# Kernel tuning notes

Hardware: AMD Instinct MI355X
Metric: run time of the kernel (lower is better)

## Reference

```python
import jax, jax.numpy as jnp
import numpy as np

B, F, DIM = 32, 2048, 1024
H, DH, Q, DEPTH, MULT = 16, 64, 64, 6, 2
INNER = H * DH  # 1024
EPS = 1e-5


def _ln(x, g, b):
    m = jnp.mean(x, axis=-1, keepdims=True)
    v = jnp.mean((x - m) ** 2, axis=-1, keepdims=True)
    return (x - m) / jnp.sqrt(v + EPS) * g + b


def setup_inputs() -> dict:
    key = jax.random.key(0)
    ks = iter(jax.random.split(key, 32))
    def rn(shape, s=0.02):
        return jax.random.normal(next(ks), shape, dtype=jnp.float32) * s
    inp = {
        "features": jax.random.normal(next(ks), (B, F, DIM), dtype=jnp.float32),
        "mask": jax.random.randint(next(ks), (B, F), 0, 2),
        "latents": jax.random.normal(next(ks), (Q, INNER), dtype=jnp.float32),
        "W_down": rn((DIM, INNER)),
        "nin_g": jnp.ones((DIM,)), "nin_b": jnp.zeros((DIM,)),
        "lf_g": jnp.ones((DEPTH, INNER)), "lf_b": jnp.zeros((DEPTH, INNER)),
        "ll_g": jnp.ones((DEPTH, INNER)), "ll_b": jnp.zeros((DEPTH, INNER)),
        "Wq": rn((DEPTH, INNER, INNER)),
        "Wk": rn((DEPTH, INNER, INNER)),
        "Wv": rn((DEPTH, INNER, INNER)),
        "ffln_g": jnp.ones((DEPTH, INNER)), "ffln_b": jnp.zeros((DEPTH, INNER)),
        "ff_w1": rn((DEPTH, INNER, MULT * INNER)),
        "ff_w2": rn((DEPTH, MULT * INNER, INNER)),
        "nout_g": jnp.ones((INNER,)), "nout_b": jnp.zeros((INNER,)),
    }
    return inp


def reference(features, mask, latents, W_down, nin_g, nin_b, lf_g, lf_b, ll_g, ll_b,
              Wq, Wk, Wv, ffln_g, ffln_b, ff_w1, ff_w2, nout_g, nout_b):
    scale = DH ** (-0.5)
    # input norm + projection down to inner_dim
    f = _ln(features, nin_g, nin_b) @ W_down            # (B, F, INNER)
    x = jnp.broadcast_to(latents, (B, Q, INNER))        # (B, Q, INNER)
    keep = (mask != 0)[:, None, None, :]                # (B, 1, 1, F)
    for i in range(DEPTH):
        xf = _ln(f, lf_g[i], lf_b[i])
        xl = _ln(x, ll_g[i], ll_b[i])
        q = (xl @ Wq[i]).reshape(B, Q, H, DH).transpose(0, 2, 1, 3) * scale  # bhqd
        k = (xf @ Wk[i]).reshape(B, F, H, DH).transpose(0, 2, 1, 3)          # bhfd
        v = (xf @ Wv[i]).reshape(B, F, H, DH).transpose(0, 2, 1, 3)          # bhfd
        sim = jnp.einsum('bhqd,bhfd->bhqf', q, k)
        sim = sim - jax.lax.stop_gradient(jnp.max(sim, axis=-1, keepdims=True))
        sim = jnp.where(keep, sim, -jnp.inf)
        alphas = jax.nn.softmax(sim, axis=-1)
        alphas = jnp.nan_to_num(alphas, nan=0.0)        # fully-masked rows -> 0
        out = jnp.einsum('bhqf,bhfd->bqhd', alphas, v).reshape(B, Q, INNER)
        # feed-forward: LN -> Linear -> ReLU -> Linear
        h = jax.nn.relu(_ln(out, ffln_g[i], ffln_b[i]) @ ff_w1[i]) @ ff_w2[i]
        x = x + h
    return _ln(x, nout_g, nout_b)
```

## Files before the change

kernel.cpp:

```cpp
#include <hip/hip_runtime.h>
#include <stdint.h>


#define DEV static __device__ __forceinline__

typedef __attribute__((ext_vector_type(8))) short short8;
typedef __attribute__((ext_vector_type(4))) float f32x4;
typedef __attribute__((ext_vector_type(4))) int int4v;
typedef __attribute__((ext_vector_type(4))) unsigned short ushort4v;
typedef unsigned short ushort_t;

DEV float bf2f(ushort_t u){ union{uint32_t i; float f;} x; x.i = ((uint32_t)u)<<16; return x.f; }
DEV ushort_t f2bf(float f){
  union{float f; uint32_t i;} x; x.f = f;
  uint32_t r = x.i + 0x7fffu + ((x.i>>16)&1u);
  return (ushort_t)(r>>16);
}

#define GLOAD16(gp, lp) __builtin_amdgcn_global_load_lds( \
    (const __attribute__((address_space(1))) uint32_t*)(gp), \
    (__attribute__((address_space(3))) uint32_t*)(lp), 16, 0, 0)

#define VMCNT(n) asm volatile("s_waitcnt vmcnt(" #n ")" ::: "memory")
#define CFENCE   asm volatile("" ::: "memory")
#define MFMA16(a,b,c) __builtin_amdgcn_mfma_f32_16x16x32_bf16(a,b,c,0,0,0)
#define MFMAI8(a,b,c) __builtin_amdgcn_mfma_i32_16x16x64_i8(a,b,c,0,0,0)

template<int NXB>
DEV void xcd_remapN(int g, int total, int& x, int& y){
  int xcd = g & 7;
  int k = g >> 3;
  int rows_per_xcd = (total / NXB) >> 3;
  y = xcd * rows_per_xcd + (k / NXB);
  x = k % NXB;
}

DEV void wreduce2(float& a, float& b){
  #pragma unroll
  for (int d = 32; d; d >>= 1){ a += __shfl_xor(a, d); b += __shfl_xor(b, d); }
}

__global__ __launch_bounds__(256) void k_compact(const int* __restrict__ mask,
                                                 int* __restrict__ idx, int* __restrict__ cnt){
  int b = blockIdx.x, t = threadIdx.x;
  const int* mb = mask + b*2048;
  int keep[8]; int c = 0;
  #pragma unroll
  for (int u = 0; u < 8; ++u){ keep[u] = (mb[t*8+u] != 0); c += keep[u]; }
  __shared__ int s[256];
  s[t] = c; __syncthreads();
  for (int off = 1; off < 256; off <<= 1){
    int v = (t >= off) ? s[t-off] : 0;
    __syncthreads();
    s[t] += v;
    __syncthreads();
  }
  int pos = s[t] - c;
  #pragma unroll
  for (int u = 0; u < 8; ++u) if (keep[u]) idx[b*2048 + pos++] = t*8 + u;
  if (t == 255) cnt[b] = s[255];
}

__global__ __launch_bounds__(256) void k_gather_norm(const float* __restrict__ feat,
        const int* __restrict__ idx, const int* __restrict__ cnt, ushort_t* __restrict__ outp){
  int w = threadIdx.x >> 6, l = threadIdx.x & 63;
  int row = blockIdx.x*4 + w;
  int b = row >> 11, j = row & 2047;
  if (j >= cnt[b]) return;
  int src = idx[b*2048 + j];
  const float* rp = feat + ((size_t)(b*2048 + src))*1024;
  float4 v[4]; float s = 0.f, q = 0.f;
  #pragma unroll
  for (int i = 0; i < 4; ++i){
    v[i] = *(const float4*)(rp + i*256 + l*4);
    s += v[i].x+v[i].y+v[i].z+v[i].w;
    q += v[i].x*v[i].x+v[i].y*v[i].y+v[i].z*v[i].z+v[i].w*v[i].w;
  }
  wreduce2(s, q);
  float mean = s * (1.f/1024.f);
  float rstd = rsqrtf(q*(1.f/1024.f) - mean*mean + 1e-5f);
  ushort_t* op = outp + (size_t)row*1024;
  #pragma unroll
  for (int i = 0; i < 4; ++i){
    ushort4v o;
    o.x = f2bf((v[i].x-mean)*rstd); o.y = f2bf((v[i].y-mean)*rstd);
    o.z = f2bf((v[i].z-mean)*rstd); o.w = f2bf((v[i].w-mean)*rstd);
    *(ushort4v*)(op + i*256 + l*4) = o;
  }
}

__global__ __launch_bounds__(256) void k_rownorm_i8(const ushort_t* __restrict__ in,
        int8_t* __restrict__ outp, float* __restrict__ sca, const int* __restrict__ cnt){
  int w = threadIdx.x >> 6, l = threadIdx.x & 63;
  int row = blockIdx.x*4 + w;
  if (cnt){ int b = row >> 11; if ((row & 2047) >= cnt[b]) return; }
  const ushort_t* rp = in + (size_t)row*1024 + l*16;
  float f[16]; float s = 0.f, q = 0.f;
  #pragma unroll
  for (int i = 0; i < 4; ++i){
    ushort4v u = *(const ushort4v*)(rp + i*4);
    f[i*4+0] = bf2f(u.x); f[i*4+1] = bf2f(u.y);
    f[i*4+2] = bf2f(u.z); f[i*4+3] = bf2f(u.w);
  }
  #pragma unroll
  for (int jj = 0; jj < 16; ++jj){ s += f[jj]; q += f[jj]*f[jj]; }
  wreduce2(s, q);
  float mean = s * (1.f/1024.f);
  float rstd = rsqrtf(q*(1.f/1024.f) - mean*mean + 1e-5f);
  float amax = 0.f;
  #pragma unroll
  for (int jj = 0; jj < 16; ++jj) amax = fmaxf(amax, fabsf(f[jj]-mean));
  #pragma unroll
  for (int d = 32; d; d >>= 1) amax = fmaxf(amax, __shfl_xor(amax, d));
  amax *= rstd;
  float inv = (amax > 0.f) ? 127.f/amax : 0.f;
  if (l == 0) sca[row] = amax * (1.f/127.f);
  uint32_t wds[4];
  #pragma unroll
  for (int i = 0; i < 4; ++i){
    uint32_t wd = 0;
    #pragma unroll
    for (int c = 0; c < 4; ++c){
      int qv = (int)rintf((f[i*4+c]-mean)*rstd*inv);
      wd |= ((uint32_t)(uint8_t)(int8_t)qv) << (c*8);
    }
    wds[i] = wd;
  }
  int4v pk; pk[0]=(int)wds[0]; pk[1]=(int)wds[1]; pk[2]=(int)wds[2]; pk[3]=(int)wds[3];
  *(int4v*)(outp + (size_t)row*1024 + l*16) = pk;
}

__global__ __launch_bounds__(256) void k_rownorm_f32_i8(const float* __restrict__ in,
        int8_t* __restrict__ outp, float* __restrict__ sca){
  int w = threadIdx.x >> 6, l = threadIdx.x & 63;
  int row = blockIdx.x*4 + w;
  const float* rp = in + (size_t)row*1024 + l*16;
  float f[16]; float s = 0.f, q = 0.f;
  #pragma unroll
  for (int i = 0; i < 4; ++i){
    float4 v = *(const float4*)(rp + i*4);
    f[i*4+0] = v.x; f[i*4+1] = v.y; f[i*4+2] = v.z; f[i*4+3] = v.w;
  }
  #pragma unroll
  for (int jj = 0; jj < 16; ++jj){ s += f[jj]; q += f[jj]*f[jj]; }
  wreduce2(s, q);
  float mean = s * (1.f/1024.f);
  float rstd = rsqrtf(q*(1.f/1024.f) - mean*mean + 1e-5f);
  float amax = 0.f;
  #pragma unroll
  for (int jj = 0; jj < 16; ++jj) amax = fmaxf(amax, fabsf(f[jj]-mean));
  #pragma unroll
  for (int d = 32; d; d >>= 1) amax = fmaxf(amax, __shfl_xor(amax, d));
  amax *= rstd;
  float inv = (amax > 0.f) ? 127.f/amax : 0.f;
  if (l == 0) sca[row] = amax * (1.f/127.f);
  uint32_t wds[4];
  #pragma unroll
  for (int i = 0; i < 4; ++i){
    uint32_t wd = 0;
    #pragma unroll
    for (int c = 0; c < 4; ++c){
      int qv = (int)rintf((f[i*4+c]-mean)*rstd*inv);
      wd |= ((uint32_t)(uint8_t)(int8_t)qv) << (c*8);
    }
    wds[i] = wd;
  }
  int4v pk; pk[0]=(int)wds[0]; pk[1]=(int)wds[1]; pk[2]=(int)wds[2]; pk[3]=(int)wds[3];
  *(int4v*)(outp + (size_t)row*1024 + l*16) = pk;
}

template<int PER>
__global__ __launch_bounds__(256) void k_quant_rows(const ushort_t* __restrict__ in,
        int8_t* __restrict__ outp, float* __restrict__ sca){
  const int K = PER*64;
  int w = threadIdx.x >> 6, l = threadIdx.x & 63;
  int row = blockIdx.x*4 + w;
  const ushort_t* rp = in + (size_t)row*K + l*PER;
  float f[PER];
  #pragma unroll
  for (int i = 0; i < PER/4; ++i){
    ushort4v u = *(const ushort4v*)(rp + i*4);
    f[i*4+0] = bf2f(u.x); f[i*4+1] = bf2f(u.y);
    f[i*4+2] = bf2f(u.z); f[i*4+3] = bf2f(u.w);
  }
  float amax = 0.f;
  #pragma unroll
  for (int jj = 0; jj < PER; ++jj) amax = fmaxf(amax, fabsf(f[jj]));
  #pragma unroll
  for (int d = 32; d; d >>= 1) amax = fmaxf(amax, __shfl_xor(amax, d));
  float inv = (amax > 0.f) ? 127.f/amax : 0.f;
  if (l == 0) sca[row] = amax * (1.f/127.f);
  #pragma unroll
  for (int vq = 0; vq < PER/16; ++vq){
    int4v pk;
    #pragma unroll
    for (int i = 0; i < 4; ++i){
      uint32_t wd = 0;
      #pragma unroll
      for (int c = 0; c < 4; ++c){
        int qv = (int)rintf(f[vq*16 + i*4 + c]*inv);
        wd |= ((uint32_t)(uint8_t)(int8_t)qv) << (c*8);
      }
      pk[i] = (int)wd;
    }
    *(int4v*)(outp + (size_t)row*K + l*PER + vq*16) = pk;
  }
}

__global__ __launch_bounds__(256) void k_final_ln(const float* __restrict__ x,
        const float* __restrict__ g, const float* __restrict__ bb, float* __restrict__ outp){
  int w = threadIdx.x >> 6, l = threadIdx.x & 63;
  int row = blockIdx.x*4 + w;
  const float* rp = x + (size_t)row*1024;
  float4 v[4]; float s = 0.f, q = 0.f;
  #pragma unroll
  for (int i = 0; i < 4; ++i){
    v[i] = *(const float4*)(rp + i*256 + l*4);
    s += v[i].x+v[i].y+v[i].z+v[i].w;
    q += v[i].x*v[i].x+v[i].y*v[i].y+v[i].z*v[i].z+v[i].w*v[i].w;
  }
  wreduce2(s, q);
  float mean = s * (1.f/1024.f);
  float rstd = rsqrtf(q*(1.f/1024.f) - mean*mean + 1e-5f);
  float* op = outp + (size_t)row*1024;
  #pragma unroll
  for (int i = 0; i < 4; ++i){
    float4 gg = *(const float4*)(g + i*256 + l*4);
    float4 bv = *(const float4*)(bb + i*256 + l*4);
    float4 o;
    o.x = (v[i].x-mean)*rstd*gg.x + bv.x; o.y = (v[i].y-mean)*rstd*gg.y + bv.y;
    o.z = (v[i].z-mean)*rstd*gg.z + bv.z; o.w = (v[i].w-mean)*rstd*gg.w + bv.w;
    *(float4*)(op + i*256 + l*4) = o;
  }
}

__global__ __launch_bounds__(256) void k_init_x(const float* __restrict__ lat, float* __restrict__ x){
  int v = blockIdx.x*256 + threadIdx.x;
  int row = v >> 8, cv = v & 255;
  ((float4*)x)[v] = ((const float4*)lat)[(row & 63)*256 + cv];
}

DEV void foldT_body(const float* __restrict__ W, const float* __restrict__ g,
                    float scale, ushort_t* __restrict__ Wt, int K, int N,
                    int n0, int k0){
  __shared__ float Ts[64][65];
  int t = threadIdx.x;
  #pragma unroll
  for (int i = 0; i < 4; ++i){
    int flat = i*1024 + t*4; int r = flat >> 6, c = flat & 63;
    float4 v = *(const float4*)(W + (size_t)(k0+r)*N + n0 + c);
    float gg = (g ? g[k0+r] : 1.f) * scale;
    Ts[r][c] = v.x*gg; Ts[r][c+1] = v.y*gg; Ts[r][c+2] = v.z*gg; Ts[r][c+3] = v.w*gg;
  }
  __syncthreads();
  #pragma unroll
  for (int i = 0; i < 4; ++i){
    int flat = i*1024 + t*4; int rn = flat >> 6, ck = flat & 63;
    ushort4v o;
    o.x = f2bf(Ts[ck][rn]);   o.y = f2bf(Ts[ck+1][rn]);
    o.z = f2bf(Ts[ck+2][rn]); o.w = f2bf(Ts[ck+3][rn]);
    *(ushort4v*)(Wt + (size_t)(n0+rn)*K + k0 + ck) = o;
  }
}

struct FDesc { const float* W; const float* g; ushort_t* dst; float scale; int K; int N; };
#define MAXFD 32
struct FoldTArgs { int cnt; FDesc d[MAXFD]; };

__global__ __launch_bounds__(256) void k_foldT_all(FoldTArgs a){
  const FDesc d = a.d[blockIdx.y];
  int nxb = d.N >> 6;
  int n0 = (blockIdx.x % nxb) * 64;
  int k0 = (blockIdx.x / nxb) * 64;
  if (k0 >= d.K) return;
  foldT_body(d.W, d.g, d.scale, d.dst, d.K, d.N, n0, k0);
}

DEV void foldBias_body(const float* __restrict__ W, const float* __restrict__ bvec,
                       float scale, float* __restrict__ bias, int K, int N, int o0){
  int t = threadIdx.x;
  int ol = t & 31, kc = t >> 5;
  int o = o0 + ol;
  int chunk = K >> 3;
  int c0 = kc*chunk, c1 = c0 + chunk;
  float s0 = 0, s1 = 0, s2 = 0, s3 = 0;
  for (int c = c0; c < c1; c += 4){
    s0 += bvec[c+0]*W[(size_t)(c+0)*N + o];
    s1 += bvec[c+1]*W[(size_t)(c+1)*N + o];
    s2 += bvec[c+2]*W[(size_t)(c+2)*N + o];
    s3 += bvec[c+3]*W[(size_t)(c+3)*N + o];
  }
  __shared__ float red[8][32];
  red[kc][ol] = (s0+s1)+(s2+s3);
  __syncthreads();
  if (kc == 0){
    float tot = 0;
    #pragma unroll
    for (int jj = 0; jj < 8; ++jj) tot += red[jj][ol];
    bias[o] = tot * scale;
  }
}

struct BDesc { const float* W; const float* b; float* dst; float scale; int K; int N; };
#define MAXBD 25
struct BiasArgs { int cnt; BDesc d[MAXBD]; };

__global__ __launch_bounds__(256) void k_foldBias_all(BiasArgs a){
  const BDesc d = a.d[blockIdx.y];
  int o0 = blockIdx.x * 32;
  if (o0 >= d.N) return;
  foldBias_body(d.W, d.b, d.scale, d.dst, d.K, d.N, o0);
}

template<int OUTMODE>
__global__ __launch_bounds__(256, 4) void k_gemm128i8(const int8_t* __restrict__ A,
        const int8_t* __restrict__ Bt, const float* __restrict__ sAr,
        const float* __restrict__ sBr, const float* __restrict__ bias,
        void* __restrict__ Cp, int M, int N, int Kb){
  const int n0 = blockIdx.x * 128;
  const int m0 = blockIdx.y * 128;
  __shared__ __align__(16) char sA[2][128*64];
  __shared__ __align__(16) char sB[2][128*64];
  const int tid = threadIdx.x;
  const int wave = tid >> 6, lane = tid & 63;
  const int lo = lane & 15, hi = lane >> 4;
  const int wr = wave >> 1, wc = wave & 1;

  auto stage = [&](int buf, int k0){
    #pragma unroll
    for (int p = 0; p < 2; ++p){
      int r = p*64 + wave*16 + (lane >> 2);
      int c = lane & 3;
      {
        const int8_t* gp = A + (size_t)(m0 + r)*Kb + k0 + c*16;
        char* lp = (char*)(&sA[buf][0]) + p*4096 + wave*1024;
        GLOAD16(gp, lp);
      }
      {
        const int8_t* gp = Bt + (size_t)(n0 + r)*Kb + k0 + c*16;
        char* lp = (char*)(&sB[buf][0]) + p*4096 + wave*1024;
        GLOAD16(gp, lp);
      }
    }
  };

  int4v acc[4][4] = {};
  stage(0, 0);
  const int nk = Kb >> 6;
  for (int ks = 0; ks < nk; ++ks){
    __syncthreads();
    if (ks + 1 < nk) stage((ks+1)&1, (ks+1) << 6);
    const int buf = ks & 1;
    int4v af[4], bfr[4];
    #pragma unroll
    for (int mi = 0; mi < 4; ++mi)
      af[mi] = *(const int4v*)(&sA[buf][(wr*64 + mi*16 + lo)*64 + hi*16]);
    #pragma unroll
    for (int ni = 0; ni < 4; ++ni)
      bfr[ni] = *(const int4v*)(&sB[buf][(wc*64 + ni*16 + lo)*64 + hi*16]);
    #pragma unroll
    for (int mi = 0; mi < 4; ++mi)
      #pragma unroll
      for (int ni = 0; ni < 4; ++ni)
        acc[mi][ni] = MFMAI8(af[mi], bfr[ni], acc[mi][ni]);
  }
  #pragma unroll
  for (int ni = 0; ni < 4; ++ni){
    int col = n0 + wc*64 + ni*16 + lo;
    float bv = bias ? bias[col] : 0.f;
    float sb = sBr[col];
    #pragma unroll
    for (int mi = 0; mi < 4; ++mi){
      int rbase = m0 + wr*64 + mi*16 + hi*4;
      #pragma unroll
      for (int rr = 0; rr < 4; ++rr){
        int row = rbase + rr;
        float v = (float)acc[mi][ni][rr] * (sAr[row]*sb) + bv;
        size_t off = (size_t)row*N + col;
        if (OUTMODE == 0)      ((ushort_t*)Cp)[off] = f2bf(v);
        else if (OUTMODE == 1) ((ushort_t*)Cp)[off] = f2bf(fmaxf(v, 0.f));
        else                   ((float*)Cp)[off] += v;
      }
    }
  }
}

template<bool SKIP, int NXB>
__global__ __launch_bounds__(512, 2) void k_gemm256p8(const ushort_t* __restrict__ A,
        const ushort_t* __restrict__ Bt, const float* __restrict__ bias,
        ushort_t* __restrict__ Cp, int M, int N, int K, const int* __restrict__ cnt){
  int bx, by;
  xcd_remapN<NXB>(blockIdx.x, gridDim.x, bx, by);
  const int n0 = bx * 256;
  const int m0 = by * 256;
  if (SKIP){ int b = m0 >> 11; if ((m0 & 2047) >= cnt[b]) return; }
  __shared__ __align__(16) ushort_t sA[2][256*64];
  __shared__ __align__(16) ushort_t sB[2][256*64];
  const int tid = threadIdx.x;
  const int wave = tid >> 6, lane = tid & 63;
  const int lo = lane & 15, hi = lane >> 4;
  const int wm = wave >> 2, wn = wave & 3;
  const int srow = lane >> 3;
  const int schunk = (lane & 7) ^ srow;
  auto stageHalf = [&](ushort_t* dst, const ushort_t* __restrict__ G, int grow0,
                       int half, int k0){
    #pragma unroll
    for (int p = 0; p < 2; ++p){
      int rbase = half*128 + p*64 + wave*8;
      const ushort_t* gp = G + (size_t)(grow0 + rbase + srow)*K + k0 + schunk*8;
      char* lp = (char*)dst + (size_t)rbase*128;
      GLOAD16(gp, lp);
    }
  };
  auto ldsA = [&](int buf, int row, int kk)->short8{
    int ch = ((kk<<2) + hi) ^ (row & 7);
    return *(const short8*)((const char*)sA + (size_t)buf*32768 + (size_t)row*128 + ch*16);
  };
  auto ldsB = [&](int buf, int row, int kk)->short8{
    int ch = ((kk<<2) + hi) ^ (row & 7);
    return *(const short8*)((const char*)sB + (size_t)buf*32768 + (size_t)row*128 + ch*16);
  };
  f32x4 acc[8][4] = {};

  short8 af[4][2], bg[2][2];
#define LOADA(BUF, AH) \
    _Pragma("unroll") for (int mi_ = 0; mi_ < 4; ++mi_) \
      _Pragma("unroll") for (int kk_ = 0; kk_ < 2; ++kk_) \
        af[mi_][kk_] = ldsA(BUF, (AH)*128 + wm*64 + mi_*16 + lo, kk_);
#define LOADB(BUF, BH) \
    _Pragma("unroll") for (int nj_ = 0; nj_ < 2; ++nj_) \
      _Pragma("unroll") for (int kk_ = 0; kk_ < 2; ++kk_) \
        bg[nj_][kk_] = ldsB(BUF, (BH)*128 + wn*32 + nj_*16 + lo, kk_);
#define MMQ(AH, BH) \
    __builtin_amdgcn_s_barrier(); CFENCE; \
    __builtin_amdgcn_s_setprio(1); \
    _Pragma("unroll") for (int mi_ = 0; mi_ < 4; ++mi_) \
      _Pragma("unroll") for (int nj_ = 0; nj_ < 2; ++nj_) \
        _Pragma("unroll") for (int kk_ = 0; kk_ < 2; ++kk_) \
          acc[(AH)*4+mi_][(BH)*2+nj_] = \
            MFMA16(af[mi_][kk_], bg[nj_][kk_], acc[(AH)*4+mi_][(BH)*2+nj_]); \
    __builtin_amdgcn_s_setprio(0); CFENCE; \
    __builtin_amdgcn_s_barrier(); CFENCE;

  stageHalf(&sA[0][0], A,  m0, 0, 0);
  stageHalf(&sB[0][0], Bt, n0, 0, 0);
  stageHalf(&sA[0][0], A,  m0, 1, 0);
  stageHalf(&sB[0][0], Bt, n0, 1, 0);
  stageHalf(&sA[1][0], A,  m0, 0, 64);
  stageHalf(&sB[1][0], Bt, n0, 1, 64);
  VMCNT(4);
  __builtin_amdgcn_s_barrier();
  CFENCE;

  const int NI = K >> 7;
  for (int i = 0; i < NI; ++i){
    const int kt = i << 7;
    const bool lastI = (i == NI-1);
    LOADA(0,0) LOADB(0,0)
    stageHalf(&sA[1][0], A,  m0, 1, kt+64);
    MMQ(0,0)
    LOADB(0,1)
    stageHalf(&sB[1][0], Bt, n0, 0, kt+64);
    MMQ(0,1)
    LOADA(0,1)
    if (!lastI) stageHalf(&sA[0][0], A,  m0, 0, kt+128);
    MMQ(1,1)
    LOADB(0,0)
    if (!lastI) stageHalf(&sB[0][0], Bt, n0, 1, kt+128);
    if (lastI){ VMCNT(0); } else { VMCNT(4); }
    MMQ(1,0)
    LOADA(1,0) LOADB(1,0)
    if (!lastI) stageHalf(&sA[0][0], A,  m0, 1, kt+128);
    MMQ(0,0)
    LOADB(1,1)
    if (!lastI) stageHalf(&sB[0][0], Bt, n0, 0, kt+128);
    MMQ(0,1)
    LOADA(1,1)
    if (!lastI) stageHalf(&sA[1][0], A,  m0, 0, kt+192);
    MMQ(1,1)
    LOADB(1,0)
    if (!lastI){ stageHalf(&sB[1][0], Bt, n0, 1, kt+192); VMCNT(4); }
    MMQ(1,0)
  }
#undef LOADA
#undef LOADB
#undef MMQ

  #pragma unroll
  for (int b2 = 0; b2 < 2; ++b2)
    #pragma unroll
    for (int nj = 0; nj < 2; ++nj){
      int col = n0 + b2*128 + wn*32 + nj*16 + lo;
      float bv = bias ? bias[col] : 0.f;
      #pragma unroll
      for (int a2 = 0; a2 < 2; ++a2)
        #pragma unroll
        for (int mi4 = 0; mi4 < 4; ++mi4){
          int rbase = m0 + a2*128 + wm*64 + mi4*16 + hi*4;
          #pragma unroll
          for (int rr = 0; rr < 4; ++rr){
            float v = acc[a2*4+mi4][b2*2+nj][rr] + bv;
            Cp[(size_t)(rbase + rr)*N + col] = f2bf(v);
          }
        }
    }
}

template<bool SKIP, int NXB>
__global__ __launch_bounds__(512, 2) void k_gemm256i8(const int8_t* __restrict__ A,
        const int8_t* __restrict__ Bt, const float* __restrict__ sAr,
        const float* __restrict__ sBr, const float* __restrict__ bias,
        ushort_t* __restrict__ Cp, int M, int N, int Kb, const int* __restrict__ cnt){
  int bx, by;
  xcd_remapN<NXB>(blockIdx.x, gridDim.x, bx, by);
  const int n0 = bx * 256;
  const int m0 = by * 256;
  if (SKIP){ int b = m0 >> 11; if ((m0 & 2047) >= cnt[b]) return; }
  __shared__ __align__(16) char sAl[2][256*128];
  __shared__ __align__(16) char sBl[2][256*128];
  const int tid = threadIdx.x;
  const int wave = tid >> 6, lane = tid & 63;
  const int lo = lane & 15, hi = lane >> 4;
  const int wm = wave >> 2, wn = wave & 3;
  const int srow = lane >> 3;
  const int schunk = (lane & 7) ^ srow;
  auto stageHalf = [&](char* dst, const int8_t* __restrict__ G, int grow0,
                       int half, int k0){
    #pragma unroll
    for (int p = 0; p < 2; ++p){
      int rbase = half*128 + p*64 + wave*8;
      const int8_t* gp = G + (size_t)(grow0 + rbase + srow)*Kb + k0 + schunk*16;
      char* lp = dst + (size_t)rbase*128;
      GLOAD16(gp, lp);
    }
  };
  auto ldsA = [&](int buf, int row, int kk)->int4v{
    int ch = ((kk<<2) + hi) ^ (row & 7);
    return *(const int4v*)((const char*)sAl + (size_t)buf*32768 + (size_t)row*128 + ch*16);
  };
  auto ldsB = [&](int buf, int row, int kk)->int4v{
    int ch = ((kk<<2) + hi) ^ (row & 7);
    return *(const int4v*)((const char*)sBl + (size_t)buf*32768 + (size_t)row*128 + ch*16);
  };
  int4v acc[8][4] = {};

  int4v af[4][2], bg[2][2];
#define LOADA(BUF, AH) \
    _Pragma("unroll") for (int mi_ = 0; mi_ < 4; ++mi_) \
      _Pragma("unroll") for (int kk_ = 0; kk_ < 2; ++kk_) \
        af[mi_][kk_] = ldsA(BUF, (AH)*128 + wm*64 + mi_*16 + lo, kk_);
#define LOADB(BUF, BH) \
    _Pragma("unroll") for (int nj_ = 0; nj_ < 2; ++nj_) \
      _Pragma("unroll") for (int kk_ = 0; kk_ < 2; ++kk_) \
        bg[nj_][kk_] = ldsB(BUF, (BH)*128 + wn*32 + nj_*16 + lo, kk_);
#define MMQ(AH, BH) \
    __builtin_amdgcn_s_barrier(); CFENCE; \
    __builtin_amdgcn_s_setprio(1); \
    _Pragma("unroll") for (int mi_ = 0; mi_ < 4; ++mi_) \
      _Pragma("unroll") for (int nj_ = 0; nj_ < 2; ++nj_) \
        _Pragma("unroll") for (int kk_ = 0; kk_ < 2; ++kk_) \
          acc[(AH)*4+mi_][(BH)*2+nj_] = \
            MFMAI8(af[mi_][kk_], bg[nj_][kk_], acc[(AH)*4+mi_][(BH)*2+nj_]); \
    __builtin_amdgcn_s_setprio(0); CFENCE; \
    __builtin_amdgcn_s_barrier(); CFENCE;

  stageHalf(&sAl[0][0], A,  m0, 0, 0);
  stageHalf(&sBl[0][0], Bt, n0, 0, 0);
  stageHalf(&sAl[0][0], A,  m0, 1, 0);
  stageHalf(&sBl[0][0], Bt, n0, 1, 0);
  stageHalf(&sAl[1][0], A,  m0, 0, 128);
  stageHalf(&sBl[1][0], Bt, n0, 1, 128);
  VMCNT(4);
  __builtin_amdgcn_s_barrier();
  CFENCE;

  const int NI = Kb >> 8;
  for (int i = 0; i < NI; ++i){
    const int kt = i << 8;
    const bool lastI = (i == NI-1);
    LOADA(0,0) LOADB(0,0)
    stageHalf(&sAl[1][0], A,  m0, 1, kt+128);
    MMQ(0,0)
    LOADB(0,1)
    stageHalf(&sBl[1][0], Bt, n0, 0, kt+128);
    MMQ(0,1)
    LOADA(0,1)
    if (!lastI) stageHalf(&sAl[0][0], A,  m0, 0, kt+256);
    MMQ(1,1)
    LOADB(0,0)
    if (!lastI) stageHalf(&sBl[0][0], Bt, n0, 1, kt+256);
    if (lastI){ VMCNT(0); } else { VMCNT(4); }
    MMQ(1,0)
    LOADA(1,0) LOADB(1,0)
    if (!lastI) stageHalf(&sAl[0][0], A,  m0, 1, kt+256);
    MMQ(0,0)
    LOADB(1,1)
    if (!lastI) stageHalf(&sBl[0][0], Bt, n0, 0, kt+256);
    MMQ(0,1)
    LOADA(1,1)
    if (!lastI) stageHalf(&sAl[1][0], A,  m0, 0, kt+384);
    MMQ(1,1)
    LOADB(1,0)
    if (!lastI){ stageHalf(&sBl[1][0], Bt, n0, 1, kt+384); VMCNT(4); }
    MMQ(1,0)
  }
#undef LOADA
#undef LOADB
#undef MMQ

  #pragma unroll
  for (int b2 = 0; b2 < 2; ++b2)
    #pragma unroll
    for (int nj = 0; nj < 2; ++nj){
      int col = n0 + b2*128 + wn*32 + nj*16 + lo;
      float bv = bias ? bias[col] : 0.f;
      float sb = sBr[col];
      #pragma unroll
      for (int a2 = 0; a2 < 2; ++a2)
        #pragma unroll
        for (int mi4 = 0; mi4 < 4; ++mi4){
          int rbase = m0 + a2*128 + wm*64 + mi4*16 + hi*4;
          #pragma unroll
          for (int rr = 0; rr < 4; ++rr){
            int row = rbase + rr;
            float v = (float)acc[a2*4+mi4][b2*2+nj][rr] * (sAr[row]*sb) + bv;
            Cp[(size_t)row*N + col] = f2bf(v);
          }
        }
    }
}

__global__ __launch_bounds__(256) void k_attn(const ushort_t* __restrict__ qb,
        const ushort_t* __restrict__ kvb, int kstride, const int* __restrict__ cnt,
        ushort_t* __restrict__ outb){
  const int bh = blockIdx.x;
  const int b = bh >> 4, h = bh & 15;
  const int t = threadIdx.x;
  const int wave = t >> 6, lane = t & 63, lo = lane & 15, hi = lane >> 4;
  __shared__ ushort_t Qs[64*64];
  __shared__ ushort_t Ks[2][64*64];
  __shared__ ushort_t Vt[2][64][72];
  __shared__ ushort_t Ps[4][16][72];

  const int count = cnt[b];

  #pragma unroll
  for (int p = 0; p < 2; ++p){
    int r = p*32 + wave*8 + (lane >> 3);
    int c = (lane & 7) ^ (r & 7);
    const ushort_t* gp = qb + (size_t)(b*64 + r)*1024 + h*64 + c*8;
    char* lp = (char*)Qs + p*4096 + wave*1024;
    GLOAD16(gp, lp);
  }

  auto stageK = [&](int buf, int tt){
    #pragma unroll
    for (int p = 0; p < 2; ++p){
      int r = p*32 + wave*8 + (lane >> 3);
      int c = (lane & 7) ^ (r & 7);
      const ushort_t* gp = kvb + (size_t)(b*2048 + tt*64 + r)*kstride + h*64 + c*8;
      char* lp = (char*)(&Ks[buf][0]) + p*4096 + wave*1024;
      GLOAD16(gp, lp);
    }
  };
  const int vjj = (t & 31)*2, vc = (t >> 5)*8;
  ushort4v va0, va1, vb0, vb1;
  auto issueV = [&](int tt){
    const ushort_t* g0 = kvb + (size_t)(b*2048 + tt*64 + vjj)*kstride + 1024 + h*64 + vc;
    va0 = *(const ushort4v*)(g0);
    va1 = *(const ushort4v*)(g0 + 4);
    vb0 = *(const ushort4v*)(g0 + kstride);
    vb1 = *(const ushort4v*)(g0 + kstride + 4);
  };
  auto writeV = [&](int buf, int tt){
    bool va  = (tt*64 + vjj)     < count;
    bool vb2 = (tt*64 + vjj + 1) < count;
    #pragma unroll
    for (int u = 0; u < 8; ++u){
      ushort_t ea = (u < 4) ? ((ushort_t*)&va0)[u] : ((ushort_t*)&va1)[u-4];
      ushort_t eb = (u < 4) ? ((ushort_t*)&vb0)[u] : ((ushort_t*)&vb1)[u-4];
      uint32_t word = (va ? (uint32_t)ea : 0u) | ((vb2 ? (uint32_t)eb : 0u) << 16);
      *(uint32_t*)(&Vt[buf][vc+u][vjj]) = word;
    }
  };

  f32x4 oacc[4] = {};
  float m[4], l[4];
  #pragma unroll
  for (int rr = 0; rr < 4; ++rr){ m[rr] = -__builtin_inff(); l[rr] = 0.f; }

  const int ntiles = (count + 63) >> 6;
  if (ntiles > 0){ stageK(0, 0); issueV(0); }

  for (int tt = 0; tt < ntiles; ++tt){
    const int buf = tt & 1;
    writeV(buf, tt);
    if (tt + 1 < ntiles){ stageK(buf^1, tt+1); issueV(tt+1); }
    asm volatile("s_waitcnt lgkmcnt(0)" ::: "memory");
    __builtin_amdgcn_s_barrier();
    CFENCE;

    f32x4 s[4] = {};
    #pragma unroll
    for (int kk = 0; kk < 2; ++kk){
      int rA = wave*16 + lo;
      short8 aq = *(const short8*)(&Qs[rA*64 + (((kk*4 + hi) ^ (rA & 7))*8)]);
      #pragma unroll
      for (int ni = 0; ni < 4; ++ni){
        int rB = ni*16 + lo;
        short8 bk = *(const short8*)(&Ks[buf][rB*64 + (((kk*4 + hi) ^ (rB & 7))*8)]);
        s[ni] = MFMA16(aq, bk, s[ni]);
      }
    }
    #pragma unroll
    for (int ni = 0; ni < 4; ++ni){
      if (tt*64 + ni*16 + lo >= count){
        s[ni][0] = s[ni][1] = s[ni][2] = s[ni][3] = -__builtin_inff();
      }
    }
    float p[4][4];
    #pragma unroll
    for (int rr = 0; rr < 4; ++rr){
      float mx = fmaxf(fmaxf(s[0][rr], s[1][rr]), fmaxf(s[2][rr], s[3][rr]));
      #pragma unroll
      for (int d = 1; d < 16; d <<= 1) mx = fmaxf(mx, __shfl_xor(mx, d));
      float mnew = fmaxf(m[rr], mx);
      float sc = __expf(m[rr] - mnew);
      float rsum = 0.f;
      #pragma unroll
      for (int ni = 0; ni < 4; ++ni){
        float pv = __expf(s[ni][rr] - mnew);
        p[ni][rr] = pv;
        rsum += pv;
      }
      #pragma unroll
      for (int d = 1; d < 16; d <<= 1) rsum += __shfl_xor(rsum, d);
      l[rr] = l[rr]*sc + rsum;
      m[rr] = mnew;
      #pragma unroll
      for (int ni = 0; ni < 4; ++ni) oacc[ni][rr] *= sc;
    }
    #pragma unroll
    for (int ni = 0; ni < 4; ++ni)
      #pragma unroll
      for (int rr = 0; rr < 4; ++rr)
        Ps[wave][hi*4+rr][ni*16+lo] = f2bf(p[ni][rr]);
    asm volatile("s_waitcnt lgkmcnt(0)" ::: "memory");
    #pragma unroll
    for (int kk = 0; kk < 2; ++kk){
      short8 pa = *(const short8*)(&Ps[wave][lo][kk*32 + hi*8]);
      #pragma unroll
      for (int ni = 0; ni < 4; ++ni){
        short8 bv = *(const short8*)(&Vt[buf][ni*16 + lo][kk*32 + hi*8]);
        oacc[ni] = MFMA16(pa, bv, oacc[ni]);
      }
    }
    CFENCE;
    __builtin_amdgcn_s_barrier();
    CFENCE;
  }
  #pragma unroll
  for (int rr = 0; rr < 4; ++rr){
    float inv = (l[rr] > 0.f) ? 1.f/l[rr] : 0.f;
    #pragma unroll
    for (int ni = 0; ni < 4; ++ni){
      size_t off = (size_t)(b*64 + wave*16 + hi*4 + rr)*1024 + h*64 + ni*16 + lo;
      outb[off] = f2bf(oacc[ni][rr] * inv);
    }
  }
}

extern "C" void kernel_launch(void* const* d_in, const int* in_sizes, int n_in,
                              void* d_out, int out_size, void* d_ws, size_t ws_size,
                              hipStream_t stream){
  const float* features = (const float*)d_in[0];
  const int*   mask     = (const int*)  d_in[1];
  const float* latents  = (const float*)d_in[2];
  const float* W_down   = (const float*)d_in[3];
  const float* nin_g    = (const float*)d_in[4];
  const float* nin_b    = (const float*)d_in[5];
  const float* lf_g     = (const float*)d_in[6];
  const float* lf_b     = (const float*)d_in[7];
  const float* ll_g     = (const float*)d_in[8];
  const float* ll_b     = (const float*)d_in[9];
  const float* Wq       = (const float*)d_in[10];
  const float* Wk       = (const float*)d_in[11];
  const float* Wv       = (const float*)d_in[12];
  const float* ffln_g   = (const float*)d_in[13];
  const float* ffln_b   = (const float*)d_in[14];
  const float* ff_w1    = (const float*)d_in[15];
  const float* ff_w2    = (const float*)d_in[16];
  const float* nout_g   = (const float*)d_in[17];
  const float* nout_b   = (const float*)d_in[18];

  char* ws = (char*)d_ws;
  size_t off = 0;
  auto alloc = [&](size_t bytes)->char*{
    char* p = ws + off;
    off += (bytes + 255) & ~(size_t)255;
    return p;
  };
  const size_t SZW = (size_t)1024*1024*2;

  ushort_t* FHAT  = (ushort_t*)alloc((size_t)65536*1024*2);
  int8_t*   I8A   = (int8_t*)  alloc((size_t)65536*1024);
  float*    SA    = (float*)   alloc((size_t)65536*4);
  int8_t*   I8KV  = (int8_t*)  alloc((size_t)12288*1024);
  float*    SKV   = (float*)   alloc((size_t)12288*4);
  int8_t*   I8Q   = (int8_t*)  alloc((size_t)6144*1024);
  float*    SQW   = (float*)   alloc((size_t)6144*4);
  int8_t*   I8W1  = (int8_t*)  alloc((size_t)12288*1024);
  float*    SW1   = (float*)   alloc((size_t)12288*4);
  int8_t*   I8W2  = (int8_t*)  alloc((size_t)6144*2048);
  float*    SW2   = (float*)   alloc((size_t)6144*4);
  ushort_t* WDT   = (ushort_t*)alloc(SZW);
  ushort_t* WQT6  = (ushort_t*)alloc(SZW*6);
  ushort_t* WKVT6 = (ushort_t*)alloc(SZW*2*6);
  ushort_t* W1T6  = (ushort_t*)alloc(SZW*2*6);
  ushort_t* W2T6  = (ushort_t*)alloc(SZW*2*6);
  float* BD   = (float*)alloc(1024*4);
  float* BQ6  = (float*)alloc(1024*4*6);
  float* BKV6 = (float*)alloc(2048*4*6);
  float* B16  = (float*)alloc(2048*4*6);
  float*    X    = (float*)   alloc((size_t)2048*1024*4);
  int8_t*   I8X  = (int8_t*)  alloc((size_t)2048*1024);
  float*    SX   = (float*)   alloc((size_t)2048*4);
  ushort_t* QP   = (ushort_t*)alloc((size_t)2048*1024*2);
  ushort_t* OUTB = (ushort_t*)alloc((size_t)2048*1024*2);
  int8_t*   I8O  = (int8_t*)  alloc((size_t)2048*1024);
  float*    SO   = (float*)   alloc((size_t)2048*4);
  ushort_t* H1   = (ushort_t*)alloc((size_t)2048*2048*2);
  int8_t*   I8H  = (int8_t*)  alloc((size_t)2048*2048);
  float*    SH   = (float*)   alloc((size_t)2048*4);
  int* CNT = (int*)alloc(32*4);
  int* IDX = (int*)alloc((size_t)65536*4);
  ushort_t* KVBUF = (ushort_t*)alloc((size_t)65536*2048*2);
  ushort_t* FNORM = KVBUF;
  (void)in_sizes; (void)n_in; (void)out_size; (void)ws_size;

  const float scale = 0.125f;

  FoldTArgs fa; int nf = 0;
  auto addF = [&](const float* W, const float* g, float sc, ushort_t* dst, int K, int N){
    fa.d[nf++] = FDesc{W, g, dst, sc, K, N};
  };
  addF(W_down, nin_g, 1.f, WDT, 1024, 1024);
  for (int i = 0; i < 6; ++i){
    const float* Wqi = Wq + (size_t)i*1024*1024;
    const float* Wki = Wk + (size_t)i*1024*1024;
    const float* Wvi = Wv + (size_t)i*1024*1024;
    const float* W1i = ff_w1 + (size_t)i*1024*2048;
    const float* W2i = ff_w2 + (size_t)i*2048*1024;
    addF(Wqi, ll_g + i*1024, scale, WQT6  + i*(SZW/2),        1024, 1024);
    addF(Wki, lf_g + i*1024, 1.f,   WKVT6 + i*SZW,            1024, 1024);
    addF(Wvi, lf_g + i*1024, 1.f,   WKVT6 + i*SZW + (SZW/2),  1024, 1024);
    addF(W1i, ffln_g + i*1024, 1.f, W1T6  + i*SZW,            1024, 2048);
    addF(W2i, nullptr, 1.f,         W2T6  + i*SZW,            2048, 1024);
  }
  fa.cnt = nf;

  BiasArgs ba; int nb = 0;
  auto addB = [&](const float* W, const float* b, float sc, float* dst, int K, int N){
    ba.d[nb++] = BDesc{W, b, dst, sc, K, N};
  };
  addB(W_down, nin_b, 1.f, BD, 1024, 1024);
  for (int i = 0; i < 6; ++i){
    const float* Wqi = Wq + (size_t)i*1024*1024;
    const float* Wki = Wk + (size_t)i*1024*1024;
    const float* Wvi = Wv + (size_t)i*1024*1024;
    const float* W1i = ff_w1 + (size_t)i*1024*2048;
    addB(Wqi, ll_b + i*1024, scale, BQ6  + i*1024,        1024, 1024);
    addB(Wki, lf_b + i*1024, 1.f,   BKV6 + i*2048,        1024, 1024);
    addB(Wvi, lf_b + i*1024, 1.f,   BKV6 + i*2048 + 1024, 1024, 1024);
    addB(W1i, ffln_b + i*1024, 1.f, B16  + i*2048,        1024, 2048);
  }
  ba.cnt = nb;

  k_compact     <<<32,    256, 0, stream>>>(mask, IDX, CNT);
  k_gather_norm <<<16384, 256, 0, stream>>>(features, IDX, CNT, FNORM);
  k_foldT_all   <<<dim3(512, nf), 256, 0, stream>>>(fa);
  k_foldBias_all<<<dim3(64,  nb), 256, 0, stream>>>(ba);
  k_quant_rows<16><<<3072, 256, 0, stream>>>(WKVT6, I8KV, SKV);
  k_quant_rows<16><<<1536, 256, 0, stream>>>(WQT6,  I8Q,  SQW);
  k_quant_rows<16><<<3072, 256, 0, stream>>>(W1T6,  I8W1, SW1);
  k_quant_rows<32><<<1536, 256, 0, stream>>>(W2T6,  I8W2, SW2);
  k_gemm256p8<true,4><<<1024, 512, 0, stream>>>(FNORM, WDT, BD, FHAT, 65536, 1024, 1024, CNT);
  k_rownorm_i8  <<<16384, 256, 0, stream>>>(FHAT, I8A, SA, CNT);
  k_init_x      <<<2048,  256, 0, stream>>>(latents, X);

  for (int i = 0; i < 6; ++i){
    k_gemm256i8<true,8><<<2048, 512, 0, stream>>>(I8A, I8KV + (size_t)i*2048*1024,
                                                  SA, SKV + i*2048, BKV6 + i*2048,
                                                  KVBUF, 65536, 2048, 1024, CNT);
    k_rownorm_f32_i8<<<512, 256, 0, stream>>>(X, I8X, SX);
    k_gemm128i8<0><<<dim3(8,16), 256, 0, stream>>>(I8X, I8Q + (size_t)i*1024*1024,
                                                   SX, SQW + i*1024, BQ6 + i*1024,
                                                   QP, 2048, 1024, 1024);
    k_attn<<<512, 256, 0, stream>>>(QP, KVBUF, 2048, CNT, OUTB);
    k_rownorm_i8<<<512, 256, 0, stream>>>(OUTB, I8O, SO, nullptr);
    k_gemm128i8<1><<<dim3(16,16), 256, 0, stream>>>(I8O, I8W1 + (size_t)i*2048*1024,
                                                    SO, SW1 + i*2048, B16 + i*2048,
                                                    H1, 2048, 2048, 1024);
    k_quant_rows<32><<<512, 256, 0, stream>>>(H1, I8H, SH);
    k_gemm128i8<2><<<dim3(8,16), 256, 0, stream>>>(I8H, I8W2 + (size_t)i*1024*2048,
                                                   SH, SW2 + i*1024, nullptr,
                                                   X, 2048, 1024, 2048);
  }
  k_final_ln<<<512, 256, 0, stream>>>(X, nout_g, nout_b, (float*)d_out);
}
```

Baseline: 1.783 ms.

## Shrink small int8 GEMM tiles and swizzle LDS layout to fill more CUs

Replaces the 128x128-tile int8 GEMM used for the latent-side Q, FF1 and FF2 projections with a templated kernel using 64-row tiles and 64- or 128-column tiles. This raises the block count from 128/256 to 512 so more of the GPU's compute units are busy on these small (M=2048) GEMMs. It also adds an XOR swizzle of 16-byte chunks in LDS to reduce bank conflicts on fragment reads. The cost is less data reuse per tile and more global traffic for the weight and activation operands.

```diff
diff --git a/kernel.cpp b/kernel.cpp
--- a/kernel.cpp
+++ b/kernel.cpp
@@ -312,66 +312,70 @@
   foldBias_body(d.W, d.b, d.scale, d.dst, d.K, d.N, o0);
 }
 
-template<int OUTMODE>
-__global__ __launch_bounds__(256, 4) void k_gemm128i8(const int8_t* __restrict__ A,
+template<int OUTMODE, int BN>
+__global__ __launch_bounds__(256, 4) void k_gemm_sm(const int8_t* __restrict__ A,
         const int8_t* __restrict__ Bt, const float* __restrict__ sAr,
         const float* __restrict__ sBr, const float* __restrict__ bias,
         void* __restrict__ Cp, int M, int N, int Kb){
-  const int n0 = blockIdx.x * 128;
-  const int m0 = blockIdx.y * 128;
-  __shared__ __align__(16) char sA[2][128*64];
-  __shared__ __align__(16) char sB[2][128*64];
+  constexpr int BM = 64;
+  constexpr int NIF = BN/32;
+  const int n0 = blockIdx.x * BN;
+  const int m0 = blockIdx.y * BM;
+  __shared__ __align__(16) char sA[2][BM*64];
+  __shared__ __align__(16) char sB[2][BN*64];
   const int tid = threadIdx.x;
   const int wave = tid >> 6, lane = tid & 63;
   const int lo = lane & 15, hi = lane >> 4;
   const int wr = wave >> 1, wc = wave & 1;
 
   auto stage = [&](int buf, int k0){
-    #pragma unroll
-    for (int p = 0; p < 2; ++p){
-      int r = p*64 + wave*16 + (lane >> 2);
-      int c = lane & 3;
-      {
-        const int8_t* gp = A + (size_t)(m0 + r)*Kb + k0 + c*16;
-        char* lp = (char*)(&sA[buf][0]) + p*4096 + wave*1024;
-        GLOAD16(gp, lp);
-      }
-      {
-        const int8_t* gp = Bt + (size_t)(n0 + r)*Kb + k0 + c*16;
-        char* lp = (char*)(&sB[buf][0]) + p*4096 + wave*1024;
-        GLOAD16(gp, lp);
-      }
-    }
-  };
-
-  int4v acc[4][4] = {};
+    {
+      int r = tid >> 2;
+      int c = (tid & 3) ^ (r & 3);
+      const int8_t* gp = A + (size_t)(m0 + r)*Kb + k0 + c*16;
+      GLOAD16(gp, &sA[buf][0] + tid*16);
+    }
+    #pragma unroll
+    for (int p = 0; p < BN/64; ++p){
+      int r = p*64 + (tid >> 2);
+      int c = (tid & 3) ^ (r & 3);
+      const int8_t* gp = Bt + (size_t)(n0 + r)*Kb + k0 + c*16;
+      GLOAD16(gp, &sB[buf][0] + p*4096 + tid*16);
+    }
+  };
+
+  int4v acc[2][NIF] = {};
   stage(0, 0);
   const int nk = Kb >> 6;
   for (int ks = 0; ks < nk; ++ks){
     __syncthreads();
     if (ks + 1 < nk) stage((ks+1)&1, (ks+1) << 6);
     const int buf = ks & 1;
-    int4v af[4], bfr[4];
-    #pragma unroll
-    for (int mi = 0; mi < 4; ++mi)
-      af[mi] = *(const int4v*)(&sA[buf][(wr*64 + mi*16 + lo)*64 + hi*16]);
-    #pragma unroll
-    for (int ni = 0; ni < 4; ++ni)
-      bfr[ni] = *(const int4v*)(&sB[buf][(wc*64 + ni*16 + lo)*64 + hi*16]);
-    #pragma unroll
-    for (int mi = 0; mi < 4; ++mi)
-      #pragma unroll
-      for (int ni = 0; ni < 4; ++ni)
+    int4v af[2], bfr[NIF];
+    #pragma unroll
+    for (int mi = 0; mi < 2; ++mi){
+      int row = wr*(BM/2) + mi*16 + lo;
+      af[mi] = *(const int4v*)(&sA[buf][row*64 + ((hi ^ (row & 3))*16)]);
+    }
+    #pragma unroll
+    for (int ni = 0; ni < NIF; ++ni){
+      int row = wc*(BN/2) + ni*16 + lo;
+      bfr[ni] = *(const int4v*)(&sB[buf][row*64 + ((hi ^ (row & 3))*16)]);
+    }
+    #pragma unroll
+    for (int mi = 0; mi < 2; ++mi)
+      #pragma unroll
+      for (int ni = 0; ni < NIF; ++ni)
         acc[mi][ni] = MFMAI8(af[mi], bfr[ni], acc[mi][ni]);
   }
   #pragma unroll
-  for (int ni = 0; ni < 4; ++ni){
-    int col = n0 + wc*64 + ni*16 + lo;
+  for (int ni = 0; ni < NIF; ++ni){
+    int col = n0 + wc*(BN/2) + ni*16 + lo;
     float bv = bias ? bias[col] : 0.f;
     float sb = sBr[col];
     #pragma unroll
-    for (int mi = 0; mi < 4; ++mi){
-      int rbase = m0 + wr*64 + mi*16 + hi*4;
+    for (int mi = 0; mi < 2; ++mi){
+      int rbase = m0 + wr*(BM/2) + mi*16 + hi*4;
       #pragma unroll
       for (int rr = 0; rr < 4; ++rr){
         int row = rbase + rr;
@@ -893,18 +897,18 @@
                                                   SA, SKV + i*2048, BKV6 + i*2048,
                                                   KVBUF, 65536, 2048, 1024, CNT);
     k_rownorm_f32_i8<<<512, 256, 0, stream>>>(X, I8X, SX);
-    k_gemm128i8<0><<<dim3(8,16), 256, 0, stream>>>(I8X, I8Q + (size_t)i*1024*1024,
-                                                   SX, SQW + i*1024, BQ6 + i*1024,
-                                                   QP, 2048, 1024, 1024);
+    k_gemm_sm<0,64><<<dim3(16,32), 256, 0, stream>>>(I8X, I8Q + (size_t)i*1024*1024,
+                                                     SX, SQW + i*1024, BQ6 + i*1024,
+                                                     QP, 2048, 1024, 1024);
     k_attn<<<512, 256, 0, stream>>>(QP, KVBUF, 2048, CNT, OUTB);
     k_rownorm_i8<<<512, 256, 0, stream>>>(OUTB, I8O, SO, nullptr);
-    k_gemm128i8<1><<<dim3(16,16), 256, 0, stream>>>(I8O, I8W1 + (size_t)i*2048*1024,
-                                                    SO, SW1 + i*2048, B16 + i*2048,
-                                                    H1, 2048, 2048, 1024);
+    k_gemm_sm<1,128><<<dim3(16,32), 256, 0, stream>>>(I8O, I8W1 + (size_t)i*2048*1024,
+                                                      SO, SW1 + i*2048, B16 + i*2048,
+                                                      H1, 2048, 2048, 1024);
     k_quant_rows<32><<<512, 256, 0, stream>>>(H1, I8H, SH);
-    k_gemm128i8<2><<<dim3(8,16), 256, 0, stream>>>(I8H, I8W2 + (size_t)i*1024*2048,
-                                                   SH, SW2 + i*1024, nullptr,
-                                                   X, 2048, 1024, 2048);
+    k_gemm_sm<2,64><<<dim3(16,32), 256, 0, stream>>>(I8H, I8W2 + (size_t)i*1024*2048,
+                                                     SH, SW2 + i*1024, nullptr,
+                                                     X, 2048, 1024, 2048);
   }
   k_final_ln<<<512, 256, 0, stream>>>(X, nout_g, nout_b, (float*)d_out);
 }
```

Measured after the change: 1.640 ms, median of 2. -8.0%, faster.
